# Optimization experiments

Measured on AMD Instinct MI355X. Metric: run time of the kernel, lower is better.

The kernel has to match this reference:

```python
import jax, jax.numpy as jnp
import numpy as np

B, T, D, S = 64, 512, 1024, 1024


def setup_inputs() -> dict:
    key = jax.random.key(0)
    k1, k2, k3, k4 = jax.random.split(key, 4)
    a = jax.random.normal(k1, (B, T, D), dtype=jnp.float32)
    s_prev = jax.random.normal(k2, (B, S), dtype=jnp.float32)
    # Dense(10, tanh) over concat dim D+S; Dense(1, relu). Glorot-ish scale.
    W1 = jax.random.normal(k3, (D + S, 10), dtype=jnp.float32) * (1.0 / np.sqrt(D + S))
    b1 = jnp.zeros((10,), dtype=jnp.float32)
    W2 = jax.random.normal(k4, (10, 1), dtype=jnp.float32) * (1.0 / np.sqrt(10))
    b2 = jnp.zeros((1,), dtype=jnp.float32)
    return {"a": a, "s_prev": s_prev, "W1": W1, "b1": b1, "W2": W2, "b2": b2}


def reference(a, s_prev, W1, b1, W2, b2):
    # RepeatVector: [B,S] -> [B,T,S]
    s_rep = jnp.broadcast_to(s_prev[:, None, :], (a.shape[0], a.shape[1], s_prev.shape[-1]))
    x = jnp.concatenate([a, s_rep], axis=-1)               # [B,T,D+S]
    h = jnp.tanh(jnp.einsum('btc,cu->btu', x, W1) + b1)    # [B,T,10]
    e = jax.nn.relu(jnp.einsum('btu,uo->bto', h, W2) + b2) # [B,T,1]
    attention_score = jax.nn.softmax(e, axis=1)            # softmax over time
    context_vector = jnp.sum(attention_score * a, axis=1, keepdims=True)  # [B,1,D]
    return context_vector, attention_score
```

## Files before the change

### kernel.cpp

```cpp
#include <hip/hip_runtime.h>

#define B_ 64
#define T_ 512
#define D_ 1024
#define S_ 1024
#define U_ 10

static constexpr int WS_PMZ = 0;
static constexpr int WS_E   = 1024;
static constexpr int WS_PV  = 33792;

template <int CTRL>
__device__ __forceinline__ float dpp_add(float x) {
    int yi = __builtin_amdgcn_update_dpp(0, __float_as_int(x), CTRL, 0xf, 0xf, true);
    return x + __int_as_float(yi);
}

__device__ __forceinline__ float wave_sum_uniform(float x) {
    x = dpp_add<0x111>(x);
    x = dpp_add<0x112>(x);
    x = dpp_add<0x114>(x);
    x = dpp_add<0x118>(x);
    x = dpp_add<0x142>(x);
    x = dpp_add<0x143>(x);
    return __int_as_float(__builtin_amdgcn_readlane(__float_as_int(x), 63));
}

__device__ __forceinline__ float uload(const float* p) {
    return __int_as_float(__builtin_amdgcn_readfirstlane(__float_as_int(*p)));
}

__global__ __launch_bounds__(256, 2) void k1_main(const float* __restrict__ a,
                                                  const float* __restrict__ s_prev,
                                                  const float* __restrict__ W1,
                                                  const float* __restrict__ b1,
                                                  const float* __restrict__ W2,
                                                  const float* __restrict__ b2,
                                                  float* __restrict__ ws) {
    const int blk  = blockIdx.x;
    const int b    = blk >> 3;
    const int p    = blk & 7;
    const int tid  = threadIdx.x;
    const int wave = tid >> 6;
    const int lane = tid & 63;

    float c[U_];
    {
        float cacc[U_];
#pragma unroll
        for (int u = 0; u < U_; u++) cacc[u] = 0.f;
#pragma unroll
        for (int r = 0; r < 4; r++) {
            const float4 s4 = *(const float4*)(s_prev + b * S_ + r * 256 + lane * 4);
            const float svv[4] = {s4.x, s4.y, s4.z, s4.w};
#pragma unroll
            for (int i = 0; i < 4; i++) {
                const int s = r * 256 + lane * 4 + i;
                const float* wp = W1 + (size_t)(D_ + s) * U_;
#pragma unroll
                for (int h = 0; h < 5; h++) {
                    float2 t = ((const float2*)wp)[h];
                    cacc[2 * h]     += svv[i] * t.x;
                    cacc[2 * h + 1] += svv[i] * t.y;
                }
            }
        }
#pragma unroll
        for (int u = 0; u < U_; u++)
            c[u] = wave_sum_uniform(cacc[u]) + uload(b1 + u);
    }

    float w2v[U_];
#pragma unroll
    for (int u = 0; u < U_; u++) w2v[u] = uload(W2 + u);
    const float b2s = uload(b2);

    float w1f[4][40];
#pragma unroll
    for (int k = 0; k < 4; k++) {
        const float* wp = W1 + (size_t)(k * 256 + lane * 4) * U_;
#pragma unroll
        for (int q = 0; q < 10; q++) {
            float4 t = ((const float4*)wp)[q];
            w1f[k][q * 4 + 0] = t.x;
            w1f[k][q * 4 + 1] = t.y;
            w1f[k][q * 4 + 2] = t.z;
            w1f[k][q * 4 + 3] = t.w;
        }
    }

    float v[4][4];
#pragma unroll
    for (int k = 0; k < 4; k++)
#pragma unroll
        for (int j = 0; j < 4; j++) v[k][j] = 0.f;
    float m = -1e30f, Z = 0.f;

    const int t0 = p * 64 + wave * 16;
    const float* abase = a + ((size_t)(b * T_ + t0)) * D_ + lane * 4;

    float4 cur[4], nxt[4];
#pragma unroll
    for (int k = 0; k < 4; k++) cur[k] = *(const float4*)(abase + k * 256);

#pragma unroll 2
    for (int tt = 0; tt < 16; tt++) {
        if (tt < 15) {
            const float* apn = abase + (size_t)(tt + 1) * D_;
#pragma unroll
            for (int k = 0; k < 4; k++) nxt[k] = *(const float4*)(apn + k * 256);
        }

        float av[4][4];
#pragma unroll
        for (int k = 0; k < 4; k++) {
            av[k][0] = cur[k].x; av[k][1] = cur[k].y;
            av[k][2] = cur[k].z; av[k][3] = cur[k].w;
        }

        float acc[U_];
#pragma unroll
        for (int u = 0; u < U_; u++) acc[u] = 0.f;
#pragma unroll
        for (int k = 0; k < 4; k++)
#pragma unroll
            for (int j = 0; j < 4; j++)
#pragma unroll
                for (int u = 0; u < U_; u++)
                    acc[u] += av[k][j] * w1f[k][j * 10 + u];

        float e = b2s;
#pragma unroll
        for (int u = 0; u < U_; u++) {
            float s = wave_sum_uniform(acc[u]);
            float x = s + c[u];
            x = fminf(fmaxf(x, -15.f), 15.f);
            float ex = __expf(2.f * x);
            float th = 1.f - 2.f * __builtin_amdgcn_rcpf(ex + 1.f);
            e += th * w2v[u];
        }
        e = fmaxf(e, 0.f);
        if (lane == 0) ws[WS_E + b * T_ + t0 + tt] = e;

        float mn = fmaxf(m, e);
        float sc = __expf(m - mn);
        float w  = __expf(e - mn);
        Z = Z * sc + w;
#pragma unroll
        for (int k = 0; k < 4; k++)
#pragma unroll
            for (int j = 0; j < 4; j++) v[k][j] = v[k][j] * sc + w * av[k][j];
        m = mn;

#pragma unroll
        for (int k = 0; k < 4; k++) cur[k] = nxt[k];
    }

    __shared__ float4 vs4[4][256];
    __shared__ float  mzs[4][2];
#pragma unroll
    for (int k = 0; k < 4; k++)
        vs4[wave][k * 64 + lane] = make_float4(v[k][0], v[k][1], v[k][2], v[k][3]);
    if (lane == 0) { mzs[wave][0] = m; mzs[wave][1] = Z; }
    __syncthreads();

    float m0 = mzs[0][0], m1 = mzs[1][0], m2 = mzs[2][0], m3 = mzs[3][0];
    float mb = fmaxf(fmaxf(m0, m1), fmaxf(m2, m3));
    float f0 = __expf(m0 - mb), f1 = __expf(m1 - mb);
    float f2 = __expf(m2 - mb), f3 = __expf(m3 - mb);
    float Zb = f0 * mzs[0][1] + f1 * mzs[1][1] + f2 * mzs[2][1] + f3 * mzs[3][1];

    float4 t0v = vs4[0][tid], t1v = vs4[1][tid], t2v = vs4[2][tid], t3v = vs4[3][tid];
    float4 o;
    o.x = f0 * t0v.x + f1 * t1v.x + f2 * t2v.x + f3 * t3v.x;
    o.y = f0 * t0v.y + f1 * t1v.y + f2 * t2v.y + f3 * t3v.y;
    o.z = f0 * t0v.z + f1 * t1v.z + f2 * t2v.z + f3 * t3v.z;
    o.w = f0 * t0v.w + f1 * t1v.w + f2 * t2v.w + f3 * t3v.w;
    ((float4*)(ws + WS_PV))[blk * 256 + tid] = o;
    if (tid == 0) { ws[WS_PMZ + blk * 2] = mb; ws[WS_PMZ + blk * 2 + 1] = Zb; }
}

__global__ __launch_bounds__(256) void k2_final(const float* __restrict__ ws,
                                                float* __restrict__ out) {
    const int b = blockIdx.x;
    const int tid = threadIdx.x;

    float pm[8], pz[8];
    float mb = -1e30f;
#pragma unroll
    for (int p = 0; p < 8; p++) {
        pm[p] = ws[WS_PMZ + (b * 8 + p) * 2];
        pz[p] = ws[WS_PMZ + (b * 8 + p) * 2 + 1];
        mb = fmaxf(mb, pm[p]);
    }
    float f[8], Z = 0.f;
#pragma unroll
    for (int p = 0; p < 8; p++) { f[p] = __expf(pm[p] - mb); Z += f[p] * pz[p]; }
    const float rz = 1.f / Z;

    float4 o = make_float4(0.f, 0.f, 0.f, 0.f);
#pragma unroll
    for (int p = 0; p < 8; p++) {
        float4 t = ((const float4*)(ws + WS_PV))[(b * 8 + p) * 256 + tid];
        o.x += f[p] * t.x; o.y += f[p] * t.y; o.z += f[p] * t.z; o.w += f[p] * t.w;
    }
    o.x *= rz; o.y *= rz; o.z *= rz; o.w *= rz;
    ((float4*)out)[b * 256 + tid] = o;

    for (int t = tid; t < T_; t += 256) {
        out[B_ * D_ + b * T_ + t] = __expf(ws[WS_E + b * T_ + t] - mb) * rz;
    }
}

extern "C" void kernel_launch(void* const* d_in, const int* in_sizes, int n_in,
                              void* d_out, int out_size, void* d_ws, size_t ws_size,
                              hipStream_t stream) {
    const float* a      = (const float*)d_in[0];
    const float* s_prev = (const float*)d_in[1];
    const float* W1     = (const float*)d_in[2];
    const float* b1     = (const float*)d_in[3];
    const float* W2     = (const float*)d_in[4];
    const float* b2     = (const float*)d_in[5];
    float* out = (float*)d_out;
    float* ws  = (float*)d_ws;

    k1_main<<<dim3(B_ * 8), dim3(256), 0, stream>>>(a, s_prev, W1, b1, W2, b2, ws);
    k2_final<<<dim3(B_), dim3(256), 0, stream>>>(ws, out);
}
```

Baseline: 208.5 us.

## Restructure score pass to one-row-per-lane with LDS async staging and two-pass softmax

Moves the s_prev·W1 bias term into a separate prep kernel and rewrites the main kernel as a single 64-lane wave per block. The wave stages `a` tiles into swizzled LDS via global_load_lds so each lane computes its own row's score with packed FMAs, removing the per-row cross-lane reductions. It then does a block-local max/sum and a second pass over `a` for the weighted sum. This removes the serial online-softmax and the DPP reduction chains, but it reads `a` twice, uses only 64 threads per block, and adds a kernel launch.

```diff
diff --git a/kernel.cpp b/kernel.cpp
--- a/kernel.cpp
+++ b/kernel.cpp
@@ -1,4 +1,5 @@
 #include <hip/hip_runtime.h>
+#include <stdint.h>
 
 #define B_ 64
 #define T_ 512
@@ -6,178 +7,201 @@
 #define S_ 1024
 #define U_ 10
 
+typedef float f32x2 __attribute__((ext_vector_type(2)));
+typedef float f32x4 __attribute__((ext_vector_type(4)));
+
 static constexpr int WS_PMZ = 0;
 static constexpr int WS_E   = 1024;
 static constexpr int WS_PV  = 33792;
+static constexpr int WS_C   = 33792 + 512 * 1024;
 
 template <int CTRL>
 __device__ __forceinline__ float dpp_add(float x) {
     int yi = __builtin_amdgcn_update_dpp(0, __float_as_int(x), CTRL, 0xf, 0xf, true);
     return x + __int_as_float(yi);
 }
-
-__device__ __forceinline__ float wave_sum_uniform(float x) {
+template <int CTRL>
+__device__ __forceinline__ float dpp_max(float x) {
+    int yi = __builtin_amdgcn_update_dpp(__float_as_int(-1e30f), __float_as_int(x),
+                                         CTRL, 0xf, 0xf, true);
+    return fmaxf(x, __int_as_float(yi));
+}
+
+__device__ __forceinline__ float wave_sum63(float x) {
     x = dpp_add<0x111>(x);
     x = dpp_add<0x112>(x);
     x = dpp_add<0x114>(x);
     x = dpp_add<0x118>(x);
     x = dpp_add<0x142>(x);
     x = dpp_add<0x143>(x);
+    return x;
+}
+__device__ __forceinline__ float wave_sum_uniform(float x) {
+    return __int_as_float(__builtin_amdgcn_readlane(__float_as_int(wave_sum63(x)), 63));
+}
+__device__ __forceinline__ float wave_max_uniform(float x) {
+    x = dpp_max<0x111>(x);
+    x = dpp_max<0x112>(x);
+    x = dpp_max<0x114>(x);
+    x = dpp_max<0x118>(x);
+    x = dpp_max<0x142>(x);
+    x = dpp_max<0x143>(x);
     return __int_as_float(__builtin_amdgcn_readlane(__float_as_int(x), 63));
 }
 
-__device__ __forceinline__ float uload(const float* p) {
-    return __int_as_float(__builtin_amdgcn_readfirstlane(__float_as_int(*p)));
-}
-
-__global__ __launch_bounds__(256, 2) void k1_main(const float* __restrict__ a,
-                                                  const float* __restrict__ s_prev,
-                                                  const float* __restrict__ W1,
-                                                  const float* __restrict__ b1,
-                                                  const float* __restrict__ W2,
-                                                  const float* __restrict__ b2,
-                                                  float* __restrict__ ws) {
+__device__ __forceinline__ f32x2 pk_fma(f32x2 a, f32x2 b, f32x2 c) {
+#if __has_builtin(__builtin_elementwise_fma)
+    return __builtin_elementwise_fma(a, b, c);
+#else
+    return a * b + c;
+#endif
+}
+
+__global__ __launch_bounds__(256) void k0_prep(const float* __restrict__ s_prev,
+                                               const float* __restrict__ W1,
+                                               const float* __restrict__ b1,
+                                               float* __restrict__ ws) {
+    const int b    = blockIdx.x;
+    const int tid  = threadIdx.x;
+    const int wave = tid >> 6;
+    const int lane = tid & 63;
+
+    f32x2 acc2[5];
+#pragma unroll
+    for (int h = 0; h < 5; h++) acc2[h] = f32x2{0.f, 0.f};
+
+    const f32x4 s4 = *(const f32x4*)(s_prev + b * S_ + tid * 4);
+    const float sv[4] = {s4.x, s4.y, s4.z, s4.w};
+#pragma unroll
+    for (int i = 0; i < 4; i++) {
+        const float* wp = W1 + (size_t)(D_ + tid * 4 + i) * U_;
+        const f32x2 svv = f32x2{sv[i], sv[i]};
+#pragma unroll
+        for (int h = 0; h < 5; h++)
+            acc2[h] = pk_fma(svv, *(const f32x2*)(wp + 2 * h), acc2[h]);
+    }
+
+    __shared__ float red[4][U_];
+    const float vals[U_] = {acc2[0].x, acc2[0].y, acc2[1].x, acc2[1].y, acc2[2].x,
+                            acc2[2].y, acc2[3].x, acc2[3].y, acc2[4].x, acc2[4].y};
+#pragma unroll
+    for (int u = 0; u < U_; u++) {
+        float s = wave_sum63(vals[u]);
+        if (lane == 63) red[wave][u] = s;
+    }
+    __syncthreads();
+    if (tid < U_)
+        ws[WS_C + b * U_ + tid] =
+            red[0][tid] + red[1][tid] + red[2][tid] + red[3][tid] + b1[tid];
+}
+
+__global__ __launch_bounds__(64) void k1_main(const float* __restrict__ a,
+                                              const float* __restrict__ W1,
+                                              const float* __restrict__ W2,
+                                              const float* __restrict__ b2,
+                                              float* __restrict__ ws) {
     const int blk  = blockIdx.x;
     const int b    = blk >> 3;
     const int p    = blk & 7;
-    const int tid  = threadIdx.x;
-    const int wave = tid >> 6;
-    const int lane = tid & 63;
-
-    float c[U_];
-    {
-        float cacc[U_];
-#pragma unroll
-        for (int u = 0; u < U_; u++) cacc[u] = 0.f;
-#pragma unroll
-        for (int r = 0; r < 4; r++) {
-            const float4 s4 = *(const float4*)(s_prev + b * S_ + r * 256 + lane * 4);
-            const float svv[4] = {s4.x, s4.y, s4.z, s4.w};
+    const int lane = threadIdx.x;
+
+    __shared__ __align__(16) float tile[2][4096];
+    __shared__ float wbuf[64];
+
+    const int t0 = p * 64;
+    const size_t arow0 = (size_t)(b * T_ + t0) * D_;
+
+    const int rs  = lane >> 4;
+    const int s15 = lane & 15;
+    int col_m[4];
+#pragma unroll
+    for (int m2 = 0; m2 < 4; m2++) col_m[m2] = s15 ^ ((4 * m2 + rs) & 15);
+
+    auto stage = [&](int buf, int sc) {
+#pragma unroll
+        for (int k = 0; k < 16; k++) {
+            const float* src =
+                a + arow0 + (size_t)(4 * k + rs) * D_ + sc * 64 + col_m[k & 3] * 4;
+            __builtin_amdgcn_global_load_lds(
+                (const __attribute__((address_space(1))) uint32_t*)src,
+                (__attribute__((address_space(3))) uint32_t*)&tile[buf][k * 256],
+                16, 0, 0);
+        }
+    };
+
+    f32x2 acc2[5];
+#pragma unroll
+    for (int h = 0; h < 5; h++) acc2[h] = f32x2{0.f, 0.f};
+
+    stage(0, 0);
+
+#pragma unroll
+    for (int sc = 0; sc < 16; sc++) {
+        if (sc < 15) {
+            stage((sc + 1) & 1, sc + 1);
+            asm volatile("s_waitcnt vmcnt(16)" ::: "memory");
+        } else {
+            asm volatile("s_waitcnt vmcnt(0)" ::: "memory");
+        }
+        __builtin_amdgcn_sched_barrier(0);
+
+        const float* tb   = &tile[sc & 1][0];
+        const float* wrow = W1 + (size_t)sc * 64 * U_;
+#pragma unroll
+        for (int j = 0; j < 16; j++) {
+            const f32x4 av = *(const f32x4*)(tb + lane * 64 + ((j ^ s15) << 2));
+            const float* wd = wrow + j * 4 * U_;
+            const float avv[4] = {av.x, av.y, av.z, av.w};
 #pragma unroll
             for (int i = 0; i < 4; i++) {
-                const int s = r * 256 + lane * 4 + i;
-                const float* wp = W1 + (size_t)(D_ + s) * U_;
-#pragma unroll
-                for (int h = 0; h < 5; h++) {
-                    float2 t = ((const float2*)wp)[h];
-                    cacc[2 * h]     += svv[i] * t.x;
-                    cacc[2 * h + 1] += svv[i] * t.y;
-                }
+                const f32x2 axx = f32x2{avv[i], avv[i]};
+#pragma unroll
+                for (int h = 0; h < 5; h++)
+                    acc2[h] = pk_fma(axx, *(const f32x2*)(wd + i * U_ + 2 * h), acc2[h]);
             }
         }
-#pragma unroll
-        for (int u = 0; u < U_; u++)
-            c[u] = wave_sum_uniform(cacc[u]) + uload(b1 + u);
-    }
-
-    float w2v[U_];
-#pragma unroll
-    for (int u = 0; u < U_; u++) w2v[u] = uload(W2 + u);
-    const float b2s = uload(b2);
-
-    float w1f[4][40];
-#pragma unroll
-    for (int k = 0; k < 4; k++) {
-        const float* wp = W1 + (size_t)(k * 256 + lane * 4) * U_;
-#pragma unroll
-        for (int q = 0; q < 10; q++) {
-            float4 t = ((const float4*)wp)[q];
-            w1f[k][q * 4 + 0] = t.x;
-            w1f[k][q * 4 + 1] = t.y;
-            w1f[k][q * 4 + 2] = t.z;
-            w1f[k][q * 4 + 3] = t.w;
-        }
-    }
-
-    float v[4][4];
-#pragma unroll
-    for (int k = 0; k < 4; k++)
-#pragma unroll
-        for (int j = 0; j < 4; j++) v[k][j] = 0.f;
-    float m = -1e30f, Z = 0.f;
-
-    const int t0 = p * 64 + wave * 16;
-    const float* abase = a + ((size_t)(b * T_ + t0)) * D_ + lane * 4;
-
-    float4 cur[4], nxt[4];
-#pragma unroll
-    for (int k = 0; k < 4; k++) cur[k] = *(const float4*)(abase + k * 256);
-
-#pragma unroll 2
-    for (int tt = 0; tt < 16; tt++) {
-        if (tt < 15) {
-            const float* apn = abase + (size_t)(tt + 1) * D_;
-#pragma unroll
-            for (int k = 0; k < 4; k++) nxt[k] = *(const float4*)(apn + k * 256);
-        }
-
-        float av[4][4];
-#pragma unroll
-        for (int k = 0; k < 4; k++) {
-            av[k][0] = cur[k].x; av[k][1] = cur[k].y;
-            av[k][2] = cur[k].z; av[k][3] = cur[k].w;
-        }
-
-        float acc[U_];
-#pragma unroll
-        for (int u = 0; u < U_; u++) acc[u] = 0.f;
-#pragma unroll
-        for (int k = 0; k < 4; k++)
-#pragma unroll
-            for (int j = 0; j < 4; j++)
-#pragma unroll
-                for (int u = 0; u < U_; u++)
-                    acc[u] += av[k][j] * w1f[k][j * 10 + u];
-
-        float e = b2s;
-#pragma unroll
-        for (int u = 0; u < U_; u++) {
-            float s = wave_sum_uniform(acc[u]);
-            float x = s + c[u];
-            x = fminf(fmaxf(x, -15.f), 15.f);
-            float ex = __expf(2.f * x);
-            float th = 1.f - 2.f * __builtin_amdgcn_rcpf(ex + 1.f);
-            e += th * w2v[u];
-        }
-        e = fmaxf(e, 0.f);
-        if (lane == 0) ws[WS_E + b * T_ + t0 + tt] = e;
-
-        float mn = fmaxf(m, e);
-        float sc = __expf(m - mn);
-        float w  = __expf(e - mn);
-        Z = Z * sc + w;
-#pragma unroll
-        for (int k = 0; k < 4; k++)
-#pragma unroll
-            for (int j = 0; j < 4; j++) v[k][j] = v[k][j] * sc + w * av[k][j];
-        m = mn;
-
-#pragma unroll
-        for (int k = 0; k < 4; k++) cur[k] = nxt[k];
-    }
-
-    __shared__ float4 vs4[4][256];
-    __shared__ float  mzs[4][2];
-#pragma unroll
-    for (int k = 0; k < 4; k++)
-        vs4[wave][k * 64 + lane] = make_float4(v[k][0], v[k][1], v[k][2], v[k][3]);
-    if (lane == 0) { mzs[wave][0] = m; mzs[wave][1] = Z; }
-    __syncthreads();
-
-    float m0 = mzs[0][0], m1 = mzs[1][0], m2 = mzs[2][0], m3 = mzs[3][0];
-    float mb = fmaxf(fmaxf(m0, m1), fmaxf(m2, m3));
-    float f0 = __expf(m0 - mb), f1 = __expf(m1 - mb);
-    float f2 = __expf(m2 - mb), f3 = __expf(m3 - mb);
-    float Zb = f0 * mzs[0][1] + f1 * mzs[1][1] + f2 * mzs[2][1] + f3 * mzs[3][1];
-
-    float4 t0v = vs4[0][tid], t1v = vs4[1][tid], t2v = vs4[2][tid], t3v = vs4[3][tid];
-    float4 o;
-    o.x = f0 * t0v.x + f1 * t1v.x + f2 * t2v.x + f3 * t3v.x;
-    o.y = f0 * t0v.y + f1 * t1v.y + f2 * t2v.y + f3 * t3v.y;
-    o.z = f0 * t0v.z + f1 * t1v.z + f2 * t2v.z + f3 * t3v.z;
-    o.w = f0 * t0v.w + f1 * t1v.w + f2 * t2v.w + f3 * t3v.w;
-    ((float4*)(ws + WS_PV))[blk * 256 + tid] = o;
-    if (tid == 0) { ws[WS_PMZ + blk * 2] = mb; ws[WS_PMZ + blk * 2 + 1] = Zb; }
+    }
+
+    const float* cb = ws + WS_C + b * U_;
+    const float xs[U_] = {acc2[0].x, acc2[0].y, acc2[1].x, acc2[1].y, acc2[2].x,
+                          acc2[2].y, acc2[3].x, acc2[3].y, acc2[4].x, acc2[4].y};
+    float e = b2[0];
+#pragma unroll
+    for (int u = 0; u < U_; u++) {
+        float x = xs[u] + cb[u];
+        float ex = exp2f(x * 2.8853900817779268f);
+        float th = 1.f - 2.f * __builtin_amdgcn_rcpf(ex + 1.f);
+        e += th * W2[u];
+    }
+    e = fmaxf(e, 0.f);
+    ws[WS_E + b * T_ + t0 + lane] = e;
+
+    const float mb = wave_max_uniform(e);
+    const float w  = exp2f((e - mb) * 1.4426950408889634f);
+    const float Zb = wave_sum_uniform(w);
+    wbuf[lane] = w;
+    asm volatile("s_waitcnt lgkmcnt(0)" ::: "memory");
+
+    f32x4 v[4];
+#pragma unroll
+    for (int q = 0; q < 4; q++) v[q] = f32x4{0.f, 0.f, 0.f, 0.f};
+
+    const float* ab = a + arow0 + lane * 4;
+#pragma unroll 8
+    for (int t = 0; t < 64; t++) {
+        const float wt = wbuf[t];
+        const float* ar = ab + (size_t)t * D_;
+#pragma unroll
+        for (int q = 0; q < 4; q++) {
+            const f32x4 av = *(const f32x4*)(ar + q * 256);
+            v[q] += wt * av;
+        }
+    }
+
+#pragma unroll
+    for (int q = 0; q < 4; q++)
+        ((f32x4*)(ws + WS_PV))[blk * 256 + q * 64 + lane] = v[q];
+    if (lane == 0) { ws[WS_PMZ + blk * 2] = mb; ws[WS_PMZ + blk * 2 + 1] = Zb; }
 }
 
 __global__ __launch_bounds__(256) void k2_final(const float* __restrict__ ws,
@@ -198,14 +222,14 @@
     for (int p = 0; p < 8; p++) { f[p] = __expf(pm[p] - mb); Z += f[p] * pz[p]; }
     const float rz = 1.f / Z;
 
-    float4 o = make_float4(0.f, 0.f, 0.f, 0.f);
+    f32x4 o = f32x4{0.f, 0.f, 0.f, 0.f};
 #pragma unroll
     for (int p = 0; p < 8; p++) {
-        float4 t = ((const float4*)(ws + WS_PV))[(b * 8 + p) * 256 + tid];
-        o.x += f[p] * t.x; o.y += f[p] * t.y; o.z += f[p] * t.z; o.w += f[p] * t.w;
-    }
-    o.x *= rz; o.y *= rz; o.z *= rz; o.w *= rz;
-    ((float4*)out)[b * 256 + tid] = o;
+        f32x4 t = ((const f32x4*)(ws + WS_PV))[(b * 8 + p) * 256 + tid];
+        o += f[p] * t;
+    }
+    o *= rz;
+    ((f32x4*)out)[b * 256 + tid] = o;
 
     for (int t = tid; t < T_; t += 256) {
         out[B_ * D_ + b * T_ + t] = __expf(ws[WS_E + b * T_ + t] - mb) * rz;
@@ -224,6 +248,7 @@
     float* out = (float*)d_out;
     float* ws  = (float*)d_ws;
 
-    k1_main<<<dim3(B_ * 8), dim3(256), 0, stream>>>(a, s_prev, W1, b1, W2, b2, ws);
+    k0_prep<<<dim3(B_), dim3(256), 0, stream>>>(s_prev, W1, b1, ws);
+    k1_main<<<dim3(B_ * 8), dim3(64), 0, stream>>>(a, W1, W2, b2, ws);
     k2_final<<<dim3(B_), dim3(256), 0, stream>>>(ws, out);
 }
```

New measurement: 358.2 us. 1.72x slower.
